# Optimization experiments

Measured on AMD Instinct MI355X. Metric: run time of the kernel, lower is better.

Reference implementation:

```python
import jax, jax.numpy as jnp
import numpy as np

NUM_CLASSES = 21
NUM_BOXES = 8732
BATCH = 128


def setup_inputs() -> dict:
    key = jax.random.key(0)
    k1, k2, k3, k4 = jax.random.split(key, 4)
    return {
        "loc_preds": jax.random.normal(k1, (BATCH, NUM_BOXES, 4), dtype=jnp.float32),
        "loc_targets": jax.random.normal(k2, (BATCH, NUM_BOXES, 4), dtype=jnp.float32),
        "conf_preds": jax.random.normal(k3, (BATCH, NUM_BOXES, NUM_CLASSES), dtype=jnp.float32),
        "label_targets": jax.random.randint(k4, (BATCH, NUM_BOXES), 0, NUM_CLASSES, dtype=jnp.int64),
    }


def reference(loc_preds, loc_targets, conf_preds, label_targets):
    n, num_boxes, _ = conf_preds.shape
    pos = label_targets > 0                                   # [n, B] matched boxes
    num_matched = jnp.sum(pos).astype(conf_preds.dtype)

    # --- localization loss: smooth L1 (beta=1) summed over positive boxes ---
    diff = loc_preds - loc_targets
    ad = jnp.abs(diff)
    sl1 = jnp.where(ad < 1.0, 0.5 * diff * diff, ad - 0.5)    # [n, B, 4]
    loc_loss = jnp.sum(jnp.where(pos[:, :, None], sl1, 0.0))

    # --- per-box CE for mining (original uses a single global max for logsumexp) ---
    x_max = jax.lax.stop_gradient(jnp.max(conf_preds))
    lse = jnp.log(jnp.sum(jnp.exp(conf_preds - x_max), axis=-1)) + x_max   # [n, B]
    gold = jnp.take_along_axis(conf_preds, label_targets[..., None], axis=-1)[..., 0]
    mining_loss = jnp.where(pos, -1.0, lse - gold)            # pos boxes forced lowest

    # --- hard negative mining: double argsort -> rank of each box's loss ---
    idx = jnp.argsort(-mining_loss, axis=1)                   # descending sort indices
    rank = jnp.argsort(idx, axis=1)                           # rank of each box
    num_pos = jnp.sum(pos.astype(jnp.int32), axis=1)          # [n]
    num_neg = jnp.minimum(3 * num_pos, num_boxes - 1)         # [n]
    neg = rank < num_neg[:, None]
    sel = pos | neg                                           # [n, B]

    # --- confidence loss: standard CE over selected boxes (F.cross_entropy) ---
    logp = jax.nn.log_softmax(conf_preds, axis=-1)
    ce = -jnp.take_along_axis(logp, label_targets[..., None], axis=-1)[..., 0]
    conf_loss = jnp.sum(jnp.where(sel, ce, 0.0))

    denom = jnp.maximum(num_matched, 1.0)
    return (loc_loss + conf_loss) / denom
```

## Files before the change

kernel.cpp:

```cpp
#include <hip/hip_runtime.h>

#define NB 8732
#define NC 21
#define BATCH 128
#define BX 35

#define WS_ROW (BATCH * BX * 4)

typedef float v4f __attribute__((ext_vector_type(4)));

__device__ inline float wred_f(float v) {
#pragma unroll
    for (int o = 32; o > 0; o >>= 1) v += __shfl_down(v, o, 64);
    return v;
}

__global__ void __launch_bounds__(256)
kA(const float* __restrict__ locp, const float* __restrict__ loct,
   const float* __restrict__ conf, const int* __restrict__ lab,
   float* __restrict__ ws) {
    __shared__ v4f xb4[4][336];
    const int r = blockIdx.y;
    const int w = threadIdx.x >> 6;
    const int ln = threadIdx.x & 63;
    const int box0 = blockIdx.x * 256 + w * 64;

    float ceS = 0.f, pceS = 0.f, llS = 0.f, npS = 0.f;

    if (box0 < NB) {
        const int cnt = min(64, NB - box0);
        const size_t rowbase = (size_t)r * NB;
        const float* __restrict__ src = conf + (rowbase + box0) * (size_t)NC;
        const v4f* __restrict__ s4 = (const v4f*)src;
        v4f* x4 = &xb4[w][0];

        int l = 0;
        v4f lp = {0.f, 0.f, 0.f, 0.f}, lt = {0.f, 0.f, 0.f, 0.f};
        if (ln < cnt) {
            const size_t box = rowbase + box0 + ln;
            l = __builtin_nontemporal_load(lab + box);
            lp = __builtin_nontemporal_load((const v4f*)(locp + box * 4));
            lt = __builtin_nontemporal_load((const v4f*)(loct + box * 4));
        }

        if (cnt == 64) {
            v4f t0 = __builtin_nontemporal_load(s4 + ln);
            v4f t1 = __builtin_nontemporal_load(s4 + 64 + ln);
            v4f t2 = __builtin_nontemporal_load(s4 + 128 + ln);
            v4f t3 = __builtin_nontemporal_load(s4 + 192 + ln);
            v4f t4 = __builtin_nontemporal_load(s4 + 256 + ln);
            v4f t5 = {0.f, 0.f, 0.f, 0.f};
            if (ln < 16) t5 = __builtin_nontemporal_load(s4 + 320 + ln);
            x4[ln] = t0;
            x4[64 + ln] = t1;
            x4[128 + ln] = t2;
            x4[192 + ln] = t3;
            x4[256 + ln] = t4;
            if (ln < 16) x4[320 + ln] = t5;
        } else {
            const int n4 = (cnt * NC) >> 2;
#pragma unroll
            for (int k = 0; k < 6; k++) {
                const int i4 = (k << 6) + ln;
                if (i4 < n4) x4[i4] = __builtin_nontemporal_load(s4 + i4);
            }
        }
        asm volatile("s_waitcnt lgkmcnt(0)" ::: "memory");

        if (ln < cnt) {
            float c[NC];
            const float* bp = (const float*)&xb4[w][0] + NC * ln;
#pragma unroll
            for (int j = 0; j < NC; j++) c[j] = bp[j];
            float m = c[0];
#pragma unroll
            for (int j = 1; j < NC; j++) m = fmaxf(m, c[j]);
            float s = 0.f;
#pragma unroll
            for (int j = 0; j < NC; j++) s += __expf(c[j] - m);
            float gold = c[0];
#pragma unroll
            for (int j = 1; j < NC; j++) gold = (j == l) ? c[j] : gold;
            const float ce = m + __logf(s) - gold;
            ceS = ce;
            if (l > 0) {
                npS = 1.f;
                pceS = ce;
                float d, ad;
                d = lp.x - lt.x; ad = fabsf(d); llS += (ad < 1.f) ? 0.5f * d * d : ad - 0.5f;
                d = lp.y - lt.y; ad = fabsf(d); llS += (ad < 1.f) ? 0.5f * d * d : ad - 0.5f;
                d = lp.z - lt.z; ad = fabsf(d); llS += (ad < 1.f) ? 0.5f * d * d : ad - 0.5f;
                d = lp.w - lt.w; ad = fabsf(d); llS += (ad < 1.f) ? 0.5f * d * d : ad - 0.5f;
            }
        }
    }

    __shared__ float sr[4][4];
    float v0 = wred_f(ceS), v1 = wred_f(pceS), v2 = wred_f(llS), v3 = wred_f(npS);
    if (ln == 0) { sr[0][w] = v0; sr[1][w] = v1; sr[2][w] = v2; sr[3][w] = v3; }
    __syncthreads();
    if (threadIdx.x == 0) {
        float A = 0, B = 0, C = 0, D = 0;
#pragma unroll
        for (int k = 0; k < 4; k++) { A += sr[0][k]; B += sr[1][k]; C += sr[2][k]; D += sr[3][k]; }
        float* slot = ws + ((size_t)r * BX + blockIdx.x) * 4;
        slot[0] = A; slot[1] = B; slot[2] = C; slot[3] = D;
    }
}

__device__ inline float ce_for_box0(const float* __restrict__ cp) {
    float c[NC];
#pragma unroll
    for (int j = 0; j < NC; j++) c[j] = cp[j];
    float m = c[0];
#pragma unroll
    for (int j = 1; j < NC; j++) m = fmaxf(m, c[j]);
    float s = 0.f;
#pragma unroll
    for (int j = 0; j < NC; j++) s += __expf(c[j] - m);
    return m + __logf(s) - c[0];
}

__global__ void __launch_bounds__(256)
kB(const float* __restrict__ conf, const int* __restrict__ lab,
   float* __restrict__ ws) {
    const int r = blockIdx.x;
    __shared__ float srow[4];
    if (threadIdx.x < 64) {
        float a = 0, b = 0, c = 0, d = 0;
        if (threadIdx.x < BX) {
            const float4 p = *(const float4*)(ws + ((size_t)r * BX + threadIdx.x) * 4);
            a = p.x; b = p.y; c = p.z; d = p.w;
        }
        a = wred_f(a); b = wred_f(b); c = wred_f(c); d = wred_f(d);
        if (threadIdx.x == 0) { srow[0] = a; srow[1] = b; srow[2] = c; srow[3] = d; }
    }
    __syncthreads();
    const float row_ce = srow[0], row_pce = srow[1], row_ll = srow[2];
    const int np = (int)srow[3];
    const int K = min(3 * np, NB - 1);
    const int nneg = NB - np;

    float rowval;
    if (K >= nneg) {
        rowval = row_ce;
    } else if (K <= 0) {
        rowval = row_pce;
    } else {
        __shared__ unsigned key[NB];
        __shared__ unsigned hist[256];
        __shared__ unsigned sb[2];
        for (int i = threadIdx.x; i < NB; i += 256) {
            const size_t box = (size_t)r * NB + i;
            unsigned k = 0u;
            if (lab[box] == 0) {
                float ce = ce_for_box0(conf + box * (size_t)NC);
                k = __float_as_uint(fmaxf(ce, 0.f));
            }
            key[i] = k;
        }
        __syncthreads();
        unsigned prefix = 0;
        int Kr = K;
        for (int round = 3; round >= 0; --round) {
            const int sh = round * 8;
            const unsigned pmask = (round == 3) ? 0u : (0xFFFFFFFFu << (8 * (round + 1)));
            for (int b = threadIdx.x; b < 256; b += 256) hist[b] = 0;
            __syncthreads();
            for (int i = threadIdx.x; i < NB; i += 256) {
                const unsigned k = key[i];
                if ((k & pmask) == prefix) atomicAdd(&hist[(k >> sh) & 255u], 1u);
            }
            __syncthreads();
            if (threadIdx.x == 0) {
                unsigned cum = 0; int b = 255;
                for (; b > 0; --b) {
                    const unsigned h = hist[b];
                    if (cum + h >= (unsigned)Kr) break;
                    cum += h;
                }
                sb[0] = cum; sb[1] = (unsigned)b;
            }
            __syncthreads();
            Kr -= (int)sb[0];
            prefix |= (sb[1] << sh);
            __syncthreads();
        }
        float local = 0.f;
        for (int i = threadIdx.x; i < NB; i += 256) {
            const unsigned k = key[i];
            if (k > prefix) local += __uint_as_float(k);
        }
        __shared__ float sred[4];
        float vv = wred_f(local);
        const int ww = threadIdx.x >> 6, lnn = threadIdx.x & 63;
        if (lnn == 0) sred[ww] = vv;
        __syncthreads();
        rowval = row_pce + sred[0] + sred[1] + sred[2] + sred[3]
               + (float)Kr * __uint_as_float(prefix);
    }

    if (threadIdx.x == 0) {
        float* o = ws + WS_ROW + r * 4;
        o[0] = rowval; o[1] = row_ll; o[2] = srow[3];
    }
}

__global__ void __launch_bounds__(256)
kC(const float* __restrict__ ws, float* __restrict__ out) {
    float cf = 0.f, lc = 0.f, nm = 0.f;
    if (threadIdx.x < BATCH) {
        const float* o = ws + WS_ROW + threadIdx.x * 4;
        cf = o[0]; lc = o[1]; nm = o[2];
    }
    __shared__ float sf[4], sl[4], sn[4];
    float vc = wred_f(cf), vl = wred_f(lc), vn = wred_f(nm);
    const int w = threadIdx.x >> 6, ln = threadIdx.x & 63;
    if (ln == 0) { sf[w] = vc; sl[w] = vl; sn[w] = vn; }
    __syncthreads();
    if (threadIdx.x == 0) {
        const float CF = sf[0] + sf[1] + sf[2] + sf[3];
        const float LC = sl[0] + sl[1] + sl[2] + sl[3];
        const float NM = sn[0] + sn[1] + sn[2] + sn[3];
        out[0] = (LC + CF) / fmaxf(NM, 1.f);
    }
}

extern "C" void kernel_launch(void* const* d_in, const int* in_sizes, int n_in,
                              void* d_out, int out_size, void* d_ws, size_t ws_size,
                              hipStream_t stream) {
    const float* locp = (const float*)d_in[0];
    const float* loct = (const float*)d_in[1];
    const float* conf = (const float*)d_in[2];
    const int* lab = (const int*)d_in[3];
    float* out = (float*)d_out;
    float* ws = (float*)d_ws;

    hipLaunchKernelGGL(kA, dim3(BX, BATCH), dim3(256), 0, stream,
                       locp, loct, conf, lab, ws);
    hipLaunchKernelGGL(kB, dim3(BATCH), dim3(256), 0, stream, conf, lab, ws);
    hipLaunchKernelGGL(kC, dim3(1), dim3(256), 0, stream, ws, out);
}
```

Before: 161.9 us.

## Fuse row selection and final reduction into main kernel via last-block atomics

Merges the three kernels into one main kernel. The last block to finish each row, found with an atomic counter, runs the radix-select hard negative mining for that row. The last row to finish then computes the final scalar. A small init kernel clears the counters, and the mining keys move from LDS to a global workspace. This removes two kernel launches and lets row selection overlap with other rows' streaming. In exchange, the radix passes now read keys from global memory/L2 instead of LDS, and the tail work is serialized onto whichever block finishes last.

```diff
diff --git a/kernel.cpp b/kernel.cpp
--- a/kernel.cpp
+++ b/kernel.cpp
@@ -6,6 +6,8 @@
 #define BX 35
 
 #define WS_ROW (BATCH * BX * 4)
+#define WS_CNT (WS_ROW + BATCH * 4)
+#define WS_KEY (WS_CNT + BATCH + 4)
 
 typedef float v4f __attribute__((ext_vector_type(4)));
 
@@ -15,11 +17,28 @@
     return v;
 }
 
+__device__ inline void pub_f(unsigned* p, float v) { atomicExch(p, __float_as_uint(v)); }
+__device__ inline float rd_f(unsigned* p) { return __uint_as_float(atomicAdd(p, 0u)); }
+
+__device__ inline float ce_for_box0(const float* __restrict__ cp) {
+    float c[NC];
+#pragma unroll
+    for (int j = 0; j < NC; j++) c[j] = cp[j];
+    float m = c[0];
+#pragma unroll
+    for (int j = 1; j < NC; j++) m = fmaxf(m, c[j]);
+    float s = 0.f;
+#pragma unroll
+    for (int j = 0; j < NC; j++) s += __expf(c[j] - m);
+    return m + __logf(s) - c[0];
+}
+
 __global__ void __launch_bounds__(256)
-kA(const float* __restrict__ locp, const float* __restrict__ loct,
+kF(const float* __restrict__ locp, const float* __restrict__ loct,
    const float* __restrict__ conf, const int* __restrict__ lab,
-   float* __restrict__ ws) {
+   float* __restrict__ ws, float* __restrict__ out) {
     __shared__ v4f xb4[4][336];
+    unsigned* wsu = (unsigned*)ws;
     const int r = blockIdx.y;
     const int w = threadIdx.x >> 6;
     const int ln = threadIdx.x & 63;
@@ -96,6 +115,7 @@
     }
 
     __shared__ float sr[4][4];
+    __shared__ int s_last;
     float v0 = wred_f(ceS), v1 = wred_f(pceS), v2 = wred_f(llS), v3 = wred_f(npS);
     if (ln == 0) { sr[0][w] = v0; sr[1][w] = v1; sr[2][w] = v2; sr[3][w] = v3; }
     __syncthreads();
@@ -103,34 +123,21 @@
         float A = 0, B = 0, C = 0, D = 0;
 #pragma unroll
         for (int k = 0; k < 4; k++) { A += sr[0][k]; B += sr[1][k]; C += sr[2][k]; D += sr[3][k]; }
-        float* slot = ws + ((size_t)r * BX + blockIdx.x) * 4;
-        slot[0] = A; slot[1] = B; slot[2] = C; slot[3] = D;
-    }
-}
-
-__device__ inline float ce_for_box0(const float* __restrict__ cp) {
-    float c[NC];
-#pragma unroll
-    for (int j = 0; j < NC; j++) c[j] = cp[j];
-    float m = c[0];
-#pragma unroll
-    for (int j = 1; j < NC; j++) m = fmaxf(m, c[j]);
-    float s = 0.f;
-#pragma unroll
-    for (int j = 0; j < NC; j++) s += __expf(c[j] - m);
-    return m + __logf(s) - c[0];
-}
-
-__global__ void __launch_bounds__(256)
-kB(const float* __restrict__ conf, const int* __restrict__ lab,
-   float* __restrict__ ws) {
-    const int r = blockIdx.x;
+        unsigned* slot = wsu + ((size_t)r * BX + blockIdx.x) * 4;
+        pub_f(slot + 0, A); pub_f(slot + 1, B); pub_f(slot + 2, C); pub_f(slot + 3, D);
+        __threadfence();
+        const unsigned old = atomicAdd(wsu + WS_CNT + r, 1u);
+        s_last = ((old % BX) == BX - 1);
+    }
+    __syncthreads();
+    if (!s_last) return;
+
     __shared__ float srow[4];
     if (threadIdx.x < 64) {
         float a = 0, b = 0, c = 0, d = 0;
         if (threadIdx.x < BX) {
-            const float4 p = *(const float4*)(ws + ((size_t)r * BX + threadIdx.x) * 4);
-            a = p.x; b = p.y; c = p.z; d = p.w;
+            unsigned* p = wsu + ((size_t)r * BX + threadIdx.x) * 4;
+            a = rd_f(p + 0); b = rd_f(p + 1); c = rd_f(p + 2); d = rd_f(p + 3);
         }
         a = wred_f(a); b = wred_f(b); c = wred_f(c); d = wred_f(d);
         if (threadIdx.x == 0) { srow[0] = a; srow[1] = b; srow[2] = c; srow[3] = d; }
@@ -147,7 +154,7 @@
     } else if (K <= 0) {
         rowval = row_pce;
     } else {
-        __shared__ unsigned key[NB];
+        unsigned* kw = wsu + WS_KEY + (size_t)r * NB;
         __shared__ unsigned hist[256];
         __shared__ unsigned sb[2];
         for (int i = threadIdx.x; i < NB; i += 256) {
@@ -157,7 +164,7 @@
                 float ce = ce_for_box0(conf + box * (size_t)NC);
                 k = __float_as_uint(fmaxf(ce, 0.f));
             }
-            key[i] = k;
+            kw[i] = k;
         }
         __syncthreads();
         unsigned prefix = 0;
@@ -168,7 +175,7 @@
             for (int b = threadIdx.x; b < 256; b += 256) hist[b] = 0;
             __syncthreads();
             for (int i = threadIdx.x; i < NB; i += 256) {
-                const unsigned k = key[i];
+                const unsigned k = kw[i];
                 if ((k & pmask) == prefix) atomicAdd(&hist[(k >> sh) & 255u], 1u);
             }
             __syncthreads();
@@ -188,7 +195,7 @@
         }
         float local = 0.f;
         for (int i = threadIdx.x; i < NB; i += 256) {
-            const unsigned k = key[i];
+            const unsigned k = kw[i];
             if (k > prefix) local += __uint_as_float(k);
         }
         __shared__ float sred[4];
@@ -200,22 +207,24 @@
                + (float)Kr * __uint_as_float(prefix);
     }
 
+    __shared__ int s_done;
     if (threadIdx.x == 0) {
-        float* o = ws + WS_ROW + r * 4;
-        o[0] = rowval; o[1] = row_ll; o[2] = srow[3];
-    }
-}
-
-__global__ void __launch_bounds__(256)
-kC(const float* __restrict__ ws, float* __restrict__ out) {
+        unsigned* o = wsu + WS_ROW + r * 4;
+        pub_f(o + 0, rowval); pub_f(o + 1, row_ll); pub_f(o + 2, srow[3]);
+        __threadfence();
+        const unsigned old = atomicAdd(wsu + WS_CNT + BATCH, 1u);
+        s_done = ((old % BATCH) == BATCH - 1);
+    }
+    __syncthreads();
+    if (!s_done) return;
+
     float cf = 0.f, lc = 0.f, nm = 0.f;
     if (threadIdx.x < BATCH) {
-        const float* o = ws + WS_ROW + threadIdx.x * 4;
-        cf = o[0]; lc = o[1]; nm = o[2];
+        unsigned* o = wsu + WS_ROW + threadIdx.x * 4;
+        cf = rd_f(o + 0); lc = rd_f(o + 1); nm = rd_f(o + 2);
     }
     __shared__ float sf[4], sl[4], sn[4];
     float vc = wred_f(cf), vl = wred_f(lc), vn = wred_f(nm);
-    const int w = threadIdx.x >> 6, ln = threadIdx.x & 63;
     if (ln == 0) { sf[w] = vc; sl[w] = vl; sn[w] = vn; }
     __syncthreads();
     if (threadIdx.x == 0) {
@@ -224,6 +233,11 @@
         const float NM = sn[0] + sn[1] + sn[2] + sn[3];
         out[0] = (LC + CF) / fmaxf(NM, 1.f);
     }
+}
+
+__global__ void __launch_bounds__(256)
+kI(unsigned* __restrict__ cnt) {
+    if (threadIdx.x < BATCH + 1) cnt[threadIdx.x] = 0u;
 }
 
 extern "C" void kernel_launch(void* const* d_in, const int* in_sizes, int n_in,
@@ -236,8 +250,7 @@
     float* out = (float*)d_out;
     float* ws = (float*)d_ws;
 
-    hipLaunchKernelGGL(kA, dim3(BX, BATCH), dim3(256), 0, stream,
-                       locp, loct, conf, lab, ws);
-    hipLaunchKernelGGL(kB, dim3(BATCH), dim3(256), 0, stream, conf, lab, ws);
-    hipLaunchKernelGGL(kC, dim3(1), dim3(256), 0, stream, ws, out);
-}
+    hipLaunchKernelGGL(kI, dim3(1), dim3(256), 0, stream, (unsigned*)ws + WS_CNT);
+    hipLaunchKernelGGL(kF, dim3(BX, BATCH), dim3(256), 0, stream,
+                       locp, loct, conf, lab, ws, out);
+}
```

Measured after the change: 368.8 us. 2.28x slower.
